# Optimization experiments

Measured on AMD Instinct MI355X. Metric: run time of the kernel, lower is better.

Reference implementation:

```python
import jax, jax.numpy as jnp
import numpy as np

H1 = 51  # lstm1 hidden size
H2 = 1   # lstm2 hidden size


def _lstm_cell(x, h, c, Wih, Whh, bih, bhh):
    # PyTorch LSTMCell: gates = x W_ih^T + b_ih + h W_hh^T + b_hh, order i,f,g,o
    gates = x @ Wih.T + h @ Whh.T + (bih + bhh)
    i, f, g, o = jnp.split(gates, 4, axis=-1)
    i = jax.nn.sigmoid(i)
    f = jax.nn.sigmoid(f)
    g = jnp.tanh(g)
    o = jax.nn.sigmoid(o)
    c_new = f * c + i * g
    h_new = o * jnp.tanh(c_new)
    return h_new, c_new


def setup_inputs() -> dict:
    key = jax.random.key(0)
    ks = jax.random.split(key, 9)
    B, T = 2048, 1024
    s1 = 1.0 / np.sqrt(H1)
    s2 = 1.0 / np.sqrt(H2)
    u = lambda k, shape, s: jax.random.uniform(k, shape, jnp.float32, -s, s)
    return {
        "input": jax.random.normal(ks[0], (B, T), dtype=jnp.float32),
        "W_ih1": u(ks[1], (4 * H1, 1), s1),
        "W_hh1": u(ks[2], (4 * H1, H1), s1),
        "b_ih1": u(ks[3], (4 * H1,), s1),
        "b_hh1": u(ks[4], (4 * H1,), s1),
        "W_ih2": u(ks[5], (4 * H2, H1), s2),
        "W_hh2": u(ks[6], (4 * H2, H2), s2),
        "b_ih2": u(ks[7], (4 * H2,), s2),
        "b_hh2": u(ks[8], (4 * H2,), s2),
        "future": 64,
    }


def reference(input, W_ih1, W_hh1, b_ih1, b_hh1, W_ih2, W_hh2, b_ih2, b_hh2, future):
    B = input.shape[0]
    dt = input.dtype
    h1 = jnp.zeros((B, H1), dt)
    c1 = jnp.zeros((B, H1), dt)
    h2 = jnp.zeros((B, H2), dt)
    c2 = jnp.zeros((B, H2), dt)

    def step(carry, x_t):
        h1, c1, h2, c2 = carry
        h1, c1 = _lstm_cell(x_t, h1, c1, W_ih1, W_hh1, b_ih1, b_hh1)
        h2, c2 = _lstm_cell(h1, h2, c2, W_ih2, W_hh2, b_ih2, b_hh2)
        return (h1, c1, h2, c2), h2

    xs = jnp.swapaxes(input, 0, 1)[:, :, None]  # [T, B, 1]
    carry, outs = jax.lax.scan(step, (h1, c1, h2, c2), xs)

    def step_future(carry, _):
        h1, c1, h2, c2 = carry
        h1, c1 = _lstm_cell(h2, h1, c1, W_ih1, W_hh1, b_ih1, b_hh1)
        h2, c2 = _lstm_cell(h1, h2, c2, W_ih2, W_hh2, b_ih2, b_hh2)
        return (h1, c1, h2, c2), h2

    if future > 0:
        _, outs_f = jax.lax.scan(step_future, carry, None, length=future)
        outs = jnp.concatenate([outs, outs_f], axis=0)

    # [T+F, B, 1] -> [B, T+F]
    return jnp.swapaxes(outs[:, :, 0], 0, 1)
```

## Files before the change

### kernel.cpp

```cpp
#include <hip/hip_runtime.h>


#define H1N  51
#define NP   26
#define WAVE 64
#define WPB  4
#define WST  54

typedef float v2f __attribute__((ext_vector_type(2)));

#define INV_LN2   1.44269504088896340736f
#define INV_LN2X2 2.88539008177792681472f

__device__ __forceinline__ float sigmoid_s(float xs) {
    return __builtin_amdgcn_rcpf(1.0f + __builtin_amdgcn_exp2f(-xs));
}
__device__ __forceinline__ float tanh_s2(float xs2) {
    float e = __builtin_amdgcn_exp2f(xs2);
    return fmaf(-2.0f, __builtin_amdgcn_rcpf(e + 1.0f), 1.0f);
}
__device__ __forceinline__ float tanh_nat(float x) {
    return tanh_s2(x * INV_LN2X2);
}
__device__ __forceinline__ float rdlane(float v, int k) {
    return __int_as_float(__builtin_amdgcn_readlane(__float_as_int(v), k));
}

__global__ __attribute__((amdgpu_flat_work_group_size(256, 256),
                          amdgpu_waves_per_eu(2)))
void lstm_seq1(const float* __restrict__ input,
               const float* __restrict__ W_ih1,
               const float* __restrict__ W_hh1,
               const float* __restrict__ b_ih1,
               const float* __restrict__ b_hh1,
               const float* __restrict__ W_ih2,
               const float* __restrict__ W_hh2,
               const float* __restrict__ b_ih2,
               const float* __restrict__ b_hh2,
               float* __restrict__ out,
               int T, int TF)
{
    const int tid = threadIdx.x;
    const int j   = tid & (WAVE - 1);
    const int wid = tid >> 6;
    const bool jv = (j < H1N);
    const int jj  = jv ? j : 0;
    const float m = jv ? 1.0f : 0.0f;
    const bool isz = (j >= H1N) && (j < H1N + 4);
    const int  q   = isz ? (j - H1N) : 0;
    const float mz = isz ? 1.0f : 0.0f;
    const float s2q = (q == 2) ? INV_LN2X2 : INV_LN2;

    const int s = blockIdx.x * WPB + wid;

    const int r_i = jj, r_f = H1N + jj, r_g = 2*H1N + jj, r_o = 3*H1N + jj;
    const float s_i = INV_LN2, s_f = INV_LN2, s_g = INV_LN2X2, s_o = INV_LN2;

    __shared__ __align__(16) float wlds[2][WAVE][WST];
    __shared__ __align__(16) float hrow[WPB][WAVE];
    __shared__ __align__(16) float zbs[WPB][4];

    v2f wI[NP], wF[NP];
#pragma unroll
    for (int kk = 0; kk < NP; ++kk) {
        const int k0 = 2*kk, k1 = k0 + 1;
        wI[kk].x = m*s_i*W_hh1[r_i*H1N + k0] + mz*s2q*W_ih2[q*H1N + k0];
        wF[kk].x = m*s_f*W_hh1[r_f*H1N + k0];
        if (k1 < H1N) {
            wI[kk].y = m*s_i*W_hh1[r_i*H1N + k1] + mz*s2q*W_ih2[q*H1N + k1];
            wF[kk].y = m*s_f*W_hh1[r_f*H1N + k1];
        } else {
            wI[kk].y = m*s_i*(b_ih1[r_i] + b_hh1[r_i]);
            wF[kk].y = m*s_f*(b_ih1[r_f] + b_hh1[r_f]);
        }
    }
#pragma unroll
    for (int kk = 0; kk < NP; ++kk)
        asm volatile("" : "+v"(wI[kk]), "+v"(wF[kk]));

    if (tid < WAVE) {
#pragma unroll
        for (int kk = 0; kk < NP; ++kk) {
            const int k0 = 2*kk, k1 = k0 + 1;
            const float g0 = m*s_g*W_hh1[r_g*H1N + k0];
            const float o0 = m*s_o*W_hh1[r_o*H1N + k0];
            float g1, o1;
            if (k1 < H1N) {
                g1 = m*s_g*W_hh1[r_g*H1N + k1];
                o1 = m*s_o*W_hh1[r_o*H1N + k1];
            } else {
                g1 = m*s_g*(b_ih1[r_g] + b_hh1[r_g]);
                o1 = m*s_o*(b_ih1[r_o] + b_hh1[r_o]);
            }
            wlds[0][j][k0] = g0; wlds[0][j][k0+1] = g1;
            wlds[1][j][k0] = o0; wlds[1][j][k0+1] = o1;
        }
    }

    const float wx_i = m*s_i*W_ih1[r_i];
    const float wx_f = m*s_f*W_ih1[r_f];
    const float wx_g = m*s_g*W_ih1[r_g];
    const float wx_o = m*s_o*W_ih1[r_o];

    const float wh2_0 = INV_LN2*W_hh2[0], wh2_1 = INV_LN2*W_hh2[1];
    const float wh2_2 = INV_LN2X2*W_hh2[2], wh2_3 = INV_LN2*W_hh2[3];
    const float b2_0 = INV_LN2*(b_ih2[0] + b_hh2[0]), b2_1 = INV_LN2*(b_ih2[1] + b_hh2[1]);
    const float b2_2 = INV_LN2X2*(b_ih2[2] + b_hh2[2]), b2_3 = INV_LN2*(b_ih2[3] + b_hh2[3]);

    hrow[wid][j] = (j == H1N) ? 1.0f : 0.0f;
    __syncthreads();

    float* __restrict__ hw  = hrow[wid];
    float* __restrict__ zbw = zbs[wid];
    const float* __restrict__ wgt = &wlds[0][j][0];
    const float* __restrict__ wot = &wlds[1][j][0];

    float c1 = 0.0f, h2 = 0.0f, c2 = 0.0f;

    const float* __restrict__ xrow = input + (long)s * T;
    float* __restrict__ orow = out + (long)s * TF;

    float xbuf = 0.0f, obuf = 0.0f;

    auto phase = [&](float xin, int xmode, int do_l2, int do_fin, int tt) {
        v2f aI = {0.0f, 0.0f}, aF = {0.0f, 0.0f};
        v2f aG = {0.0f, 0.0f}, aO = {0.0f, 0.0f};
#pragma unroll
        for (int kk = 0; kk < NP; ++kk) {
            const v2f hp = *(const v2f*)&hw[2*kk];
            const v2f gk = *(const v2f*)&wgt[2*kk];
            const v2f ok = *(const v2f*)&wot[2*kk];
            asm("v_pk_fma_f32 %0, %4, %8, %0\n\t"
                "v_pk_fma_f32 %1, %5, %8, %1\n\t"
                "v_pk_fma_f32 %2, %6, %8, %2\n\t"
                "v_pk_fma_f32 %3, %7, %8, %3"
                : "+v"(aI), "+v"(aF), "+v"(aG), "+v"(aO)
                : "v"(wI[kk]), "v"(wF[kk]), "v"(gk), "v"(ok), "v"(hp));
        }
        const float mI = aI.x + aI.y;
        if (isz) zbw[q] = mI;
        const float mF = aF.x + aF.y, mG = aG.x + aG.y, mO = aO.x + aO.y;

        if (do_l2) {
            const float4 z = *(const float4*)zbw;
            const float g2i = sigmoid_s(fmaf(wh2_0, h2, b2_0 + z.x));
            const float g2f = sigmoid_s(fmaf(wh2_1, h2, b2_1 + z.y));
            const float g2g = tanh_s2 (fmaf(wh2_2, h2, b2_2 + z.z));
            const float g2o = sigmoid_s(fmaf(wh2_3, h2, b2_3 + z.w));
            c2 = fmaf(g2f, c2, g2i * g2g);
            h2 = g2o * tanh_nat(c2);
            obuf = (j == (tt & 63)) ? h2 : obuf;
        }
        if (do_fin) {
            const float x = (xmode == 0) ? xin : h2;
            const float gi = sigmoid_s(fmaf(wx_i, x, mI));
            const float gf = sigmoid_s(fmaf(wx_f, x, mF));
            const float gg = tanh_s2 (fmaf(wx_g, x, mG));
            const float go = sigmoid_s(fmaf(wx_o, x, mO));
            c1 = fmaf(gf, c1, gi * gg);
            const float h1 = go * tanh_nat(c1);
            if (jv) hw[j] = h1;
        }
    };

    xbuf = xrow[j];
    phase(rdlane(xbuf, 0), 0, 0, 1, 0);

    for (int n = 1; n < T; ++n) {
        if ((n & 63) == 0) xbuf = xrow[n + j];
        const float x = rdlane(xbuf, n & 63);
        phase(x, 0, 1, 1, n - 1);
        if ((n & 63) == 0) orow[n - 64 + j] = obuf;
    }

    phase(0.0f, 1, 1, 1, T - 1);
    orow[T - 64 + j] = obuf;

    for (int n = T + 1; n < TF; ++n)
        phase(0.0f, 1, 1, 1, n - 1);

    phase(0.0f, 1, 1, 0, TF - 1);
    orow[TF - 64 + j] = obuf;
}

extern "C" void kernel_launch(void* const* d_in, const int* in_sizes, int n_in,
                              void* d_out, int out_size, void* d_ws, size_t ws_size,
                              hipStream_t stream) {
    const float* input = (const float*)d_in[0];
    const float* W_ih1 = (const float*)d_in[1];
    const float* W_hh1 = (const float*)d_in[2];
    const float* b_ih1 = (const float*)d_in[3];
    const float* b_hh1 = (const float*)d_in[4];
    const float* W_ih2 = (const float*)d_in[5];
    const float* W_hh2 = (const float*)d_in[6];
    const float* b_ih2 = (const float*)d_in[7];
    const float* b_hh2 = (const float*)d_in[8];
    float* out = (float*)d_out;

    const int B  = 2048;
    const int T  = in_sizes[0] / B;
    const int TF = out_size   / B;

    lstm_seq1<<<dim3(B / WPB), dim3(WPB * WAVE), 0, stream>>>(
        input, W_ih1, W_hh1, b_ih1, b_hh1, W_ih2, W_hh2, b_ih2, b_hh2,
        out, T, TF);
}
```

Baseline: 1.210 ms.

## Keep all four gate weight sets in registers with one-wave blocks

Moves the g and o gate weights of W_hh1 out of LDS and into VGPRs, so each wave holds all four gate weight vectors in registers. Blocks shrink to a single wave per sequence, which removes the shared weight table and the block-wide barrier. The hidden state is now read from LDS as float4 instead of float2. Doubling the per-thread weight registers limits waves per SIMD and could cause spills, so latency hiding may suffer.

```diff
diff --git a/kernel.cpp b/kernel.cpp
--- a/kernel.cpp
+++ b/kernel.cpp
@@ -3,11 +3,11 @@
 
 #define H1N  51
 #define NP   26
+#define NQ   13
 #define WAVE 64
-#define WPB  4
-#define WST  54
 
 typedef float v2f __attribute__((ext_vector_type(2)));
+typedef float v4f __attribute__((ext_vector_type(4)));
 
 #define INV_LN2   1.44269504088896340736f
 #define INV_LN2X2 2.88539008177792681472f
@@ -26,23 +26,21 @@
     return __int_as_float(__builtin_amdgcn_readlane(__float_as_int(v), k));
 }
 
-__global__ __attribute__((amdgpu_flat_work_group_size(256, 256),
+__global__ __attribute__((amdgpu_flat_work_group_size(64, 64),
                           amdgpu_waves_per_eu(2)))
-void lstm_seq1(const float* __restrict__ input,
-               const float* __restrict__ W_ih1,
-               const float* __restrict__ W_hh1,
-               const float* __restrict__ b_ih1,
-               const float* __restrict__ b_hh1,
-               const float* __restrict__ W_ih2,
-               const float* __restrict__ W_hh2,
-               const float* __restrict__ b_ih2,
-               const float* __restrict__ b_hh2,
-               float* __restrict__ out,
-               int T, int TF)
+void lstm_seq1r(const float* __restrict__ input,
+                const float* __restrict__ W_ih1,
+                const float* __restrict__ W_hh1,
+                const float* __restrict__ b_ih1,
+                const float* __restrict__ b_hh1,
+                const float* __restrict__ W_ih2,
+                const float* __restrict__ W_hh2,
+                const float* __restrict__ b_ih2,
+                const float* __restrict__ b_hh2,
+                float* __restrict__ out,
+                int T, int TF)
 {
-    const int tid = threadIdx.x;
-    const int j   = tid & (WAVE - 1);
-    const int wid = tid >> 6;
+    const int j   = threadIdx.x;
     const bool jv = (j < H1N);
     const int jj  = jv ? j : 0;
     const float m = jv ? 1.0f : 0.0f;
@@ -51,51 +49,37 @@
     const float mz = isz ? 1.0f : 0.0f;
     const float s2q = (q == 2) ? INV_LN2X2 : INV_LN2;
 
-    const int s = blockIdx.x * WPB + wid;
+    const int s = blockIdx.x;
 
     const int r_i = jj, r_f = H1N + jj, r_g = 2*H1N + jj, r_o = 3*H1N + jj;
     const float s_i = INV_LN2, s_f = INV_LN2, s_g = INV_LN2X2, s_o = INV_LN2;
 
-    __shared__ __align__(16) float wlds[2][WAVE][WST];
-    __shared__ __align__(16) float hrow[WPB][WAVE];
-    __shared__ __align__(16) float zbs[WPB][4];
+    __shared__ __align__(16) float hrow[WAVE];
+    __shared__ __align__(16) float zb[4];
 
-    v2f wI[NP], wF[NP];
+    v2f wI[NP], wF[NP], wG[NP], wO[NP];
 #pragma unroll
     for (int kk = 0; kk < NP; ++kk) {
         const int k0 = 2*kk, k1 = k0 + 1;
         wI[kk].x = m*s_i*W_hh1[r_i*H1N + k0] + mz*s2q*W_ih2[q*H1N + k0];
         wF[kk].x = m*s_f*W_hh1[r_f*H1N + k0];
+        wG[kk].x = m*s_g*W_hh1[r_g*H1N + k0];
+        wO[kk].x = m*s_o*W_hh1[r_o*H1N + k0];
         if (k1 < H1N) {
             wI[kk].y = m*s_i*W_hh1[r_i*H1N + k1] + mz*s2q*W_ih2[q*H1N + k1];
             wF[kk].y = m*s_f*W_hh1[r_f*H1N + k1];
+            wG[kk].y = m*s_g*W_hh1[r_g*H1N + k1];
+            wO[kk].y = m*s_o*W_hh1[r_o*H1N + k1];
         } else {
             wI[kk].y = m*s_i*(b_ih1[r_i] + b_hh1[r_i]);
             wF[kk].y = m*s_f*(b_ih1[r_f] + b_hh1[r_f]);
+            wG[kk].y = m*s_g*(b_ih1[r_g] + b_hh1[r_g]);
+            wO[kk].y = m*s_o*(b_ih1[r_o] + b_hh1[r_o]);
         }
     }
 #pragma unroll
     for (int kk = 0; kk < NP; ++kk)
-        asm volatile("" : "+v"(wI[kk]), "+v"(wF[kk]));
-
-    if (tid < WAVE) {
-#pragma unroll
-        for (int kk = 0; kk < NP; ++kk) {
-            const int k0 = 2*kk, k1 = k0 + 1;
-            const float g0 = m*s_g*W_hh1[r_g*H1N + k0];
-            const float o0 = m*s_o*W_hh1[r_o*H1N + k0];
-            float g1, o1;
-            if (k1 < H1N) {
-                g1 = m*s_g*W_hh1[r_g*H1N + k1];
-                o1 = m*s_o*W_hh1[r_o*H1N + k1];
-            } else {
-                g1 = m*s_g*(b_ih1[r_g] + b_hh1[r_g]);
-                o1 = m*s_o*(b_ih1[r_o] + b_hh1[r_o]);
-            }
-            wlds[0][j][k0] = g0; wlds[0][j][k0+1] = g1;
-            wlds[1][j][k0] = o0; wlds[1][j][k0+1] = o1;
-        }
-    }
+        asm volatile("" : "+v"(wI[kk]), "+v"(wF[kk]), "+v"(wG[kk]), "+v"(wO[kk]));
 
     const float wx_i = m*s_i*W_ih1[r_i];
     const float wx_f = m*s_f*W_ih1[r_f];
@@ -107,13 +91,7 @@
     const float b2_0 = INV_LN2*(b_ih2[0] + b_hh2[0]), b2_1 = INV_LN2*(b_ih2[1] + b_hh2[1]);
     const float b2_2 = INV_LN2X2*(b_ih2[2] + b_hh2[2]), b2_3 = INV_LN2*(b_ih2[3] + b_hh2[3]);
 
-    hrow[wid][j] = (j == H1N) ? 1.0f : 0.0f;
-    __syncthreads();
-
-    float* __restrict__ hw  = hrow[wid];
-    float* __restrict__ zbw = zbs[wid];
-    const float* __restrict__ wgt = &wlds[0][j][0];
-    const float* __restrict__ wot = &wlds[1][j][0];
+    hrow[j] = (j == H1N) ? 1.0f : 0.0f;
 
     float c1 = 0.0f, h2 = 0.0f, c2 = 0.0f;
 
@@ -126,23 +104,31 @@
         v2f aI = {0.0f, 0.0f}, aF = {0.0f, 0.0f};
         v2f aG = {0.0f, 0.0f}, aO = {0.0f, 0.0f};
 #pragma unroll
-        for (int kk = 0; kk < NP; ++kk) {
-            const v2f hp = *(const v2f*)&hw[2*kk];
-            const v2f gk = *(const v2f*)&wgt[2*kk];
-            const v2f ok = *(const v2f*)&wot[2*kk];
+        for (int kq = 0; kq < NQ; ++kq) {
+            const v4f h4 = *(const v4f*)&hrow[4*kq];
+            const v2f hp0 = __builtin_shufflevector(h4, h4, 0, 1);
+            const v2f hp1 = __builtin_shufflevector(h4, h4, 2, 3);
             asm("v_pk_fma_f32 %0, %4, %8, %0\n\t"
                 "v_pk_fma_f32 %1, %5, %8, %1\n\t"
                 "v_pk_fma_f32 %2, %6, %8, %2\n\t"
                 "v_pk_fma_f32 %3, %7, %8, %3"
                 : "+v"(aI), "+v"(aF), "+v"(aG), "+v"(aO)
-                : "v"(wI[kk]), "v"(wF[kk]), "v"(gk), "v"(ok), "v"(hp));
+                : "v"(wI[2*kq]), "v"(wF[2*kq]), "v"(wG[2*kq]), "v"(wO[2*kq]),
+                  "v"(hp0));
+            asm("v_pk_fma_f32 %0, %4, %8, %0\n\t"
+                "v_pk_fma_f32 %1, %5, %8, %1\n\t"
+                "v_pk_fma_f32 %2, %6, %8, %2\n\t"
+                "v_pk_fma_f32 %3, %7, %8, %3"
+                : "+v"(aI), "+v"(aF), "+v"(aG), "+v"(aO)
+                : "v"(wI[2*kq+1]), "v"(wF[2*kq+1]), "v"(wG[2*kq+1]), "v"(wO[2*kq+1]),
+                  "v"(hp1));
         }
         const float mI = aI.x + aI.y;
-        if (isz) zbw[q] = mI;
+        if (isz) zb[q] = mI;
         const float mF = aF.x + aF.y, mG = aG.x + aG.y, mO = aO.x + aO.y;
 
         if (do_l2) {
-            const float4 z = *(const float4*)zbw;
+            const float4 z = *(const float4*)zb;
             const float g2i = sigmoid_s(fmaf(wh2_0, h2, b2_0 + z.x));
             const float g2f = sigmoid_s(fmaf(wh2_1, h2, b2_1 + z.y));
             const float g2g = tanh_s2 (fmaf(wh2_2, h2, b2_2 + z.z));
@@ -159,7 +145,7 @@
             const float go = sigmoid_s(fmaf(wx_o, x, mO));
             c1 = fmaf(gf, c1, gi * gg);
             const float h1 = go * tanh_nat(c1);
-            if (jv) hw[j] = h1;
+            if (jv) hrow[j] = h1;
         }
     };
 
@@ -201,7 +187,7 @@
     const int T  = in_sizes[0] / B;
     const int TF = out_size   / B;
 
-    lstm_seq1<<<dim3(B / WPB), dim3(WPB * WAVE), 0, stream>>>(
+    lstm_seq1r<<<dim3(B), dim3(WAVE), 0, stream>>>(
         input, W_ih1, W_hh1, b_ih1, b_hh1, W_ih2, W_hh2, b_ih2, b_hh2,
         out, T, TF);
 }
```

New measurement: 1.058 ms. 1.14x faster.
